# Kernel optimization log

Hardware: AMD Instinct MI355X
Metric: run time of the kernel (lower is better)

Reference implementation:

```python
import jax, jax.numpy as jnp
import numpy as np

B, S, D = 8, 1024, 768
H = 12
DH = D // H  # 64


def setup_inputs() -> dict:
    key = jax.random.key(0)
    ks = jax.random.split(key, 9)
    s = 0.02
    return {
        "x": jax.random.normal(ks[0], (B, S, D), dtype=jnp.float32),
        # per-head QKV projections stacked over heads: [H, D, DH]
        "Wq": jax.random.normal(ks[1], (H, D, DH), dtype=jnp.float32) * s,
        "bq": jax.random.normal(ks[2], (H, DH), dtype=jnp.float32) * s,
        "Wk": jax.random.normal(ks[3], (H, D, DH), dtype=jnp.float32) * s,
        "bk": jax.random.normal(ks[4], (H, DH), dtype=jnp.float32) * s,
        "Wv": jax.random.normal(ks[5], (H, D, DH), dtype=jnp.float32) * s,
        "bv": jax.random.normal(ks[6], (H, DH), dtype=jnp.float32) * s,
        # output projection: [D, D] (applied as x @ Wo + bo)
        "Wo": jax.random.normal(ks[7], (D, D), dtype=jnp.float32) * s,
        "bo": jax.random.normal(ks[8], (D,), dtype=jnp.float32) * s,
    }


def reference(x, Wq, bq, Wk, bk, Wv, bv, Wo, bo):
    # Per-head linear projections, vectorized over heads -> [B, H, S, DH]
    q = jnp.einsum("bsd,hde->bhse", x, Wq) + bq[None, :, None, :]
    k = jnp.einsum("bsd,hde->bhse", x, Wk) + bk[None, :, None, :]
    v = jnp.einsum("bsd,hde->bhse", x, Wv) + bv[None, :, None, :]
    scale = 1.0 / jnp.sqrt(jnp.asarray(DH, dtype=q.dtype))
    scores = jnp.einsum("bhse,bhte->bhst", q, k) * scale  # [B,H,S,S]
    probs = jax.nn.softmax(scores, axis=-1)  # dropout p=0 (eval)
    out = jnp.einsum("bhst,bhte->bhse", probs, v)  # [B,H,S,DH]
    # concat heads (head order matches ModuleList order) -> [B,S,D]
    out = out.transpose(0, 2, 1, 3).reshape(B, S, D)
    return out @ Wo + bo
```

## Files before the change

### kernel.cpp

```cpp
#include <hip/hip_runtime.h>
#include <math.h>

#define BB 8
#define SS 1024
#define DD 768
#define HH 12
#define DHH 64
#define BSS (BB*SS)
#define NQKV 2304
#define NT 24

typedef _Float16 half8 __attribute__((ext_vector_type(8)));
typedef _Float16 half4 __attribute__((ext_vector_type(4)));
typedef float    f32x4 __attribute__((ext_vector_type(4)));

__device__ __forceinline__ void glds16(const _Float16* g, _Float16* l)
{
    __builtin_amdgcn_global_load_lds(
        (const __attribute__((address_space(1))) uint32_t*)(g),
        (__attribute__((address_space(3))) uint32_t*)(l),
        16, 0, 0);
}

#define MF(a, b, c) __builtin_amdgcn_mfma_f32_16x16x32_f16(a, b, c, 0, 0, 0)

__global__ __launch_bounds__(256)
void prep(const float* __restrict__ x, _Float16* __restrict__ xh,
          const float* __restrict__ Wq, const float* __restrict__ Wk,
          const float* __restrict__ Wv, const float* __restrict__ Wo,
          _Float16* __restrict__ Wt, _Float16* __restrict__ Wot)
{
    const int blk = blockIdx.x;
    const int tid = threadIdx.x;

    if (blk < 3072) {
        int i = blk * 256 + tid;
        const float4* xp = (const float4*)x + (size_t)i * 2;
        float4 u = xp[0], v = xp[1];
        half8 h = { (_Float16)u.x, (_Float16)u.y, (_Float16)u.z, (_Float16)u.w,
                    (_Float16)v.x, (_Float16)v.y, (_Float16)v.z, (_Float16)v.w };
        ((half8*)xh)[i] = h;
        return;
    }

    __shared__ float T[64][65];
    const int t  = blk - 3072;
    const int z  = t / 144;
    const int r_ = t - z * 144;
    const int d0 = (r_ / 12) * 64;
    const int n_outer = r_ % 12;

    const float* src;
    _Float16* dst;
    int base_mul, row_stride;
    if (z < 3) {
        src = (z == 0) ? Wq : (z == 1) ? Wk : Wv;
        dst = Wt + (size_t)z * DD * DD;
        base_mul = DD * DHH; row_stride = DHH;
    } else {
        src = Wo; dst = Wot;
        base_mul = 64; row_stride = DD;
    }

    const size_t base = (size_t)n_outer * base_mul;
    {
        int dl = tid >> 2, c0 = (tid & 3) * 16;
        const float* p = src + base + (size_t)(d0 + dl) * row_stride + c0;
#pragma unroll
        for (int m = 0; m < 4; ++m) {
            float4 f = *(const float4*)(p + m * 4);
            T[dl][c0 + m*4 + 0] = f.x;
            T[dl][c0 + m*4 + 1] = f.y;
            T[dl][c0 + m*4 + 2] = f.z;
            T[dl][c0 + m*4 + 3] = f.w;
        }
    }
    __syncthreads();
    {
        int e = tid >> 2, c = tid & 3;
        half8 lo, hi;
#pragma unroll
        for (int i = 0; i < 8; ++i) {
            lo[i] = (_Float16)T[c*16 + i][e];
            hi[i] = (_Float16)T[c*16 + 8 + i][e];
        }
        _Float16* q = dst + ((size_t)n_outer * 64 + e) * DD + d0 + c * 16;
        *(half8*)q = lo;
        *(half8*)(q + 8) = hi;
    }
}

__global__ __launch_bounds__(512, 2)
void gemm_qkv_256(const _Float16* __restrict__ Xh, const _Float16* __restrict__ Wt,
                  const float* __restrict__ bq, const float* __restrict__ bk,
                  const float* __restrict__ bv,
                  _Float16* __restrict__ qo, _Float16* __restrict__ ko,
                  _Float16* __restrict__ vto)
{
    __shared__ _Float16 Ab[4][256][32];
    __shared__ _Float16 Bb[4][256][32];

    const int bid = blockIdx.x;
    const int c = bid & 7;
    const int g = bid >> 3;
    const int m0 = (c * 4 + g / 9) * 256;
    const int n0 = (g % 9) * 256;

    const int tid  = threadIdx.x;
    const int wave = tid >> 6;
    const int lane = tid & 63;
    const int l16  = tid & 15;
    const int quad = (tid >> 4) & 3;
    const int wy = wave >> 2;
    const int wx = wave & 3;

    const int scol = ((lane & 3) ^ ((lane >> 3) & 3)) * 8;
    const _Float16* ap0 = Xh + (size_t)(m0 + wave * 32 + (lane >> 2)) * DD + scol;
    const _Float16* bp0 = Wt + (size_t)(n0 + wave * 32 + (lane >> 2)) * DD + scol;

    const int fcol = (quad ^ ((l16 >> 1) & 3)) * 8;

    f32x4 acc[8][4];
#pragma unroll
    for (int i = 0; i < 8; ++i)
#pragma unroll
        for (int j = 0; j < 4; ++j) acc[i][j] = (f32x4){0.f, 0.f, 0.f, 0.f};

#pragma unroll
    for (int t = 0; t < 3; ++t) {
        glds16(ap0 + t * 32,           &Ab[t][wave * 32][0]);
        glds16(ap0 + t * 32 + 16 * DD, &Ab[t][wave * 32 + 16][0]);
        glds16(bp0 + t * 32,           &Bb[t][wave * 32][0]);
        glds16(bp0 + t * 32 + 16 * DD, &Bb[t][wave * 32 + 16][0]);
    }
    asm volatile("s_waitcnt vmcnt(8)\n\ts_barrier" ::: "memory");

#pragma unroll 4
    for (int kt = 0; kt < NT; ++kt) {
        const int bf = kt & 3;

        half8 a[8], bA[2];
#pragma unroll
        for (int i = 0; i < 8; ++i)
            a[i] = *(const half8*)&Ab[bf][wy * 128 + i * 16 + l16][fcol];
#pragma unroll
        for (int j = 0; j < 2; ++j)
            bA[j] = *(const half8*)&Bb[bf][wx * 64 + j * 16 + l16][fcol];
        if (kt + 3 < NT) {
            const int nf = (kt + 3) & 3;
            glds16(ap0 + (kt + 3) * 32,           &Ab[nf][wave * 32][0]);
            glds16(ap0 + (kt + 3) * 32 + 16 * DD, &Ab[nf][wave * 32 + 16][0]);
        }
        __builtin_amdgcn_s_setprio(1);
#pragma unroll
        for (int i = 0; i < 8; ++i) {
            acc[i][0] = MF(a[i], bA[0], acc[i][0]);
            acc[i][1] = MF(a[i], bA[1], acc[i][1]);
        }
        __builtin_amdgcn_s_setprio(0);

        half8 bB[2];
#pragma unroll
        for (int j = 0; j < 2; ++j)
            bB[j] = *(const half8*)&Bb[bf][wx * 64 + (2 + j) * 16 + l16][fcol];
        if (kt + 3 < NT) {
            const int nf = (kt + 3) & 3;
            glds16(bp0 + (kt + 3) * 32,           &Bb[nf][wave * 32][0]);
            glds16(bp0 + (kt + 3) * 32 + 16 * DD, &Bb[nf][wave * 32 + 16][0]);
        }
        __builtin_amdgcn_s_setprio(1);
#pragma unroll
        for (int i = 0; i < 8; ++i) {
            acc[i][2] = MF(a[i], bB[0], acc[i][2]);
            acc[i][3] = MF(a[i], bB[1], acc[i][3]);
        }
        __builtin_amdgcn_s_setprio(0);

        if (kt < NT - 3)
            asm volatile("s_waitcnt vmcnt(8)\n\ts_barrier" ::: "memory");
        else if (kt == NT - 3)
            asm volatile("s_waitcnt vmcnt(4)\n\ts_barrier" ::: "memory");
        else if (kt == NT - 2)
            asm volatile("s_waitcnt vmcnt(0)\n\ts_barrier" ::: "memory");
    }

    const int wsel  = n0 / 768;
    const int ncol0 = n0 - wsel * 768 + wx * 64;

    if (wsel == 0) {
#pragma unroll
        for (int i = 0; i < 8; ++i) {
#pragma unroll
            for (int r = 0; r < 4; ++r) {
                int row = m0 + wy * 128 + i * 16 + quad * 4 + r;
                int b_ = row >> 10;
                int s  = row & (SS - 1);
#pragma unroll
                for (int j = 0; j < 4; ++j) {
                    int nl = ncol0 + j * 16 + l16;
                    int h = nl >> 6, e = nl & 63;
                    float val = (acc[i][j][r] + bq[nl]) * 0.125f;
                    qo[((size_t)(b_ * HH + h) * SS + s) * DHH + e] = (_Float16)val;
                }
            }
        }
    } else if (wsel == 1) {
#pragma unroll
        for (int i = 0; i < 8; ++i) {
#pragma unroll
            for (int r = 0; r < 4; ++r) {
                int row = m0 + wy * 128 + i * 16 + quad * 4 + r;
                int b_ = row >> 10;
                int s  = row & (SS - 1);
#pragma unroll
                for (int j = 0; j < 4; ++j) {
                    int nl = ncol0 + j * 16 + l16;
                    int h = nl >> 6, e = nl & 63;
                    float val = acc[i][j][r] + bk[nl];
                    ko[((size_t)(b_ * HH + h) * SS + s) * DHH + e] = (_Float16)val;
                }
            }
        }
    } else {
#pragma unroll
        for (int i = 0; i < 8; ++i) {
#pragma unroll
            for (int r = 0; r < 4; ++r) {
                int row = m0 + wy * 128 + i * 16 + quad * 4 + r;
                int b_ = row >> 10;
                int s  = row & (SS - 1);
#pragma unroll
                for (int j = 0; j < 4; ++j) {
                    int nl = ncol0 + j * 16 + l16;
                    int h = nl >> 6, e = nl & 63;
                    float val = acc[i][j][r] + bv[nl];
                    vto[((size_t)(b_ * HH + h) * DHH + e) * SS + s] = (_Float16)val;
                }
            }
        }
    }
}

__global__ __launch_bounds__(256)
void gemm_out_f16(const _Float16* __restrict__ Ah, const _Float16* __restrict__ Bt,
                  const float* __restrict__ bias, float* __restrict__ out)
{
    __shared__ _Float16 Ash[2][128][32];
    __shared__ _Float16 Bsh[2][64][32];

    const int m0 = blockIdx.x * 128;
    const int n0 = blockIdx.y * 64;
    const int tid  = threadIdx.x;
    const int wave = tid >> 6;
    const int lane = tid & 63;
    const int l16  = tid & 15;
    const int quad = (tid >> 4) & 3;
    const int wy = wave >> 1;
    const int wx = wave & 1;

    const int scol = ((lane & 3) ^ ((lane >> 3) & 3)) * 8;
    const int fcol = (quad ^ ((l16 >> 1) & 3)) * 8;

    const _Float16* ap = Ah + (size_t)(m0 + 32 * wave + (lane >> 2)) * DD + scol;
    const _Float16* bp = Bt + (size_t)(n0 + 16 * wave + (lane >> 2)) * DD + scol;

    f32x4 acc[4][2];
#pragma unroll
    for (int i = 0; i < 4; ++i)
#pragma unroll
        for (int j = 0; j < 2; ++j) acc[i][j] = (f32x4){0.f, 0.f, 0.f, 0.f};

    glds16(ap, &Ash[0][32 * wave][0]);
    glds16(ap + 16 * DD, &Ash[0][32 * wave + 16][0]);
    glds16(bp, &Bsh[0][16 * wave][0]);

    int cur = 0;
    for (int k0 = 0; k0 < DD; k0 += 32) {
        __syncthreads();
        if (k0 + 32 < DD) {
            glds16(ap + k0 + 32, &Ash[cur ^ 1][32 * wave][0]);
            glds16(ap + k0 + 32 + 16 * DD, &Ash[cur ^ 1][32 * wave + 16][0]);
            glds16(bp + k0 + 32, &Bsh[cur ^ 1][16 * wave][0]);
        }

        half8 a[4], bf[2];
#pragma unroll
        for (int i = 0; i < 4; ++i)
            a[i] = *(const half8*)&Ash[cur][wy * 64 + i * 16 + l16][fcol];
#pragma unroll
        for (int j = 0; j < 2; ++j)
            bf[j] = *(const half8*)&Bsh[cur][wx * 32 + j * 16 + l16][fcol];
#pragma unroll
        for (int i = 0; i < 4; ++i)
#pragma unroll
            for (int j = 0; j < 2; ++j)
                acc[i][j] = MF(a[i], bf[j], acc[i][j]);
        cur ^= 1;
    }

#pragma unroll
    for (int i = 0; i < 4; ++i) {
#pragma unroll
        for (int r = 0; r < 4; ++r) {
            int row = m0 + wy * 64 + i * 16 + quad * 4 + r;
#pragma unroll
            for (int j = 0; j < 2; ++j) {
                int col = n0 + wx * 32 + j * 16 + l16;
                out[(size_t)row * DD + col] = acc[i][j][r] + bias[col];
            }
        }
    }
}

__global__ __launch_bounds__(256)
void attn_f16(const _Float16* __restrict__ qh, const _Float16* __restrict__ kh,
              const _Float16* __restrict__ vt, _Float16* __restrict__ ctxh)
{
    const int bh  = blockIdx.x;
    const int q0  = blockIdx.y * 128;
    const int tid = threadIdx.x;
    const int wave = tid >> 6;
    const int lane = tid & 63;
    const int l16  = tid & 15;
    const int quad = (tid >> 4) & 3;

    __shared__ _Float16 Ks[2][2][64][32];
    __shared__ _Float16 Vs[2][2][64][32];
    __shared__ _Float16 Pt[4][32][72];

    const int scol = ((lane & 3) ^ ((lane >> 3) & 3)) * 8;
    const int fcol = (quad ^ ((l16 >> 1) & 3)) * 8;

    const _Float16* qrow0 = qh + ((size_t)bh * SS + q0 + wave * 32 + l16) * DHH;
    const half8 qlo0 = *(const half8*)(qrow0 + quad * 8);
    const half8 qhi0 = *(const half8*)(qrow0 + 32 + quad * 8);
    const half8 qlo1 = *(const half8*)(qrow0 + 16 * DHH + quad * 8);
    const half8 qhi1 = *(const half8*)(qrow0 + 16 * DHH + 32 + quad * 8);

    const _Float16* kp = kh + ((size_t)bh * SS + 16 * wave + (lane >> 2)) * DHH + scol;
    const _Float16* vp = vt + ((size_t)bh * DHH + 16 * wave + (lane >> 2)) * SS + scol;

    f32x4 o0[4], o1[4];
    float lacc0 = 0.f, lacc1 = 0.f;
#pragma unroll
    for (int j = 0; j < 4; ++j) {
        o0[j] = (f32x4){0.f, 0.f, 0.f, 0.f};
        o1[j] = (f32x4){0.f, 0.f, 0.f, 0.f};
    }

    glds16(kp,      &Ks[0][0][16 * wave][0]);
    glds16(kp + 32, &Ks[0][1][16 * wave][0]);
    glds16(vp,      &Vs[0][0][16 * wave][0]);
    glds16(vp + 32, &Vs[0][1][16 * wave][0]);

    int cur = 0;
    for (int kt = 0; kt < SS; kt += 64) {
        __syncthreads();
        if (kt + 64 < SS) {
            glds16(kp + (size_t)(kt + 64) * DHH,      &Ks[cur ^ 1][0][16 * wave][0]);
            glds16(kp + (size_t)(kt + 64) * DHH + 32, &Ks[cur ^ 1][1][16 * wave][0]);
            glds16(vp + kt + 64,      &Vs[cur ^ 1][0][16 * wave][0]);
            glds16(vp + kt + 64 + 32, &Vs[cur ^ 1][1][16 * wave][0]);
        }

        f32x4 z0[4], z1[4];
#pragma unroll
        for (int f = 0; f < 4; ++f) {
            half8 klo = *(const half8*)&Ks[cur][0][f * 16 + l16][fcol];
            half8 khi = *(const half8*)&Ks[cur][1][f * 16 + l16][fcol];
            z0[f] = (f32x4){0.f, 0.f, 0.f, 0.f};
            z0[f] = MF(klo, qlo0, z0[f]);
            z0[f] = MF(khi, qhi0, z0[f]);
            z1[f] = (f32x4){0.f, 0.f, 0.f, 0.f};
            z1[f] = MF(klo, qlo1, z1[f]);
            z1[f] = MF(khi, qhi1, z1[f]);
        }

        half8 vv0[4], vv1[4];
#pragma unroll
        for (int j = 0; j < 4; ++j) {
            vv0[j] = *(const half8*)&Vs[cur][0][j * 16 + l16][fcol];
            vv1[j] = *(const half8*)&Vs[cur][1][j * 16 + l16][fcol];
        }

#pragma unroll
        for (int f = 0; f < 4; ++f) {
            half4 pk0, pk1;
#pragma unroll
            for (int r = 0; r < 4; ++r) {
                float p0 = __expf(z0[f][r]); lacc0 += p0; pk0[r] = (_Float16)p0;
                float p1 = __expf(z1[f][r]); lacc1 += p1; pk1[r] = (_Float16)p1;
            }
            *(half4*)&Pt[wave][l16][f * 16 + quad * 4]      = pk0;
            *(half4*)&Pt[wave][16 + l16][f * 16 + quad * 4] = pk1;
        }

        half8 pl0 = *(const half8*)&Pt[wave][l16][quad * 8];
        half8 ph0 = *(const half8*)&Pt[wave][l16][32 + quad * 8];
        half8 pl1 = *(const half8*)&Pt[wave][16 + l16][quad * 8];
        half8 ph1 = *(const half8*)&Pt[wave][16 + l16][32 + quad * 8];

#pragma unroll
        for (int j = 0; j < 4; ++j) {
            o0[j] = MF(pl0, vv0[j], o0[j]);
            o0[j] = MF(ph0, vv1[j], o0[j]);
            o1[j] = MF(pl1, vv0[j], o1[j]);
            o1[j] = MF(ph1, vv1[j], o1[j]);
        }
        cur ^= 1;
    }

    float lr0 = lacc0;
    lr0 += __shfl_xor(lr0, 16);
    lr0 += __shfl_xor(lr0, 32);
    float lr1 = lacc1;
    lr1 += __shfl_xor(lr1, 16);
    lr1 += __shfl_xor(lr1, 32);

    const int b_ = bh / HH;
    const int h_ = bh % HH;
#pragma unroll
    for (int r = 0; r < 4; ++r) {
        float inv0 = 1.f / __shfl(lr0, quad * 4 + r, 16);
        float inv1 = 1.f / __shfl(lr1, quad * 4 + r, 16);
        int s0_ = q0 + wave * 32 + quad * 4 + r;
        _Float16* orow0 = ctxh + ((size_t)(b_ * SS + s0_)) * DD + h_ * DHH;
        _Float16* orow1 = ctxh + ((size_t)(b_ * SS + s0_ + 16)) * DD + h_ * DHH;
#pragma unroll
        for (int j = 0; j < 4; ++j) {
            orow0[j * 16 + l16] = (_Float16)(o0[j][r] * inv0);
            orow1[j * 16 + l16] = (_Float16)(o1[j][r] * inv1);
        }
    }
}

extern "C" void kernel_launch(void* const* d_in, const int* in_sizes, int n_in,
                              void* d_out, int out_size, void* d_ws, size_t ws_size,
                              hipStream_t stream)
{
    const float* x  = (const float*)d_in[0];
    const float* Wq = (const float*)d_in[1];
    const float* bq = (const float*)d_in[2];
    const float* Wk = (const float*)d_in[3];
    const float* bk = (const float*)d_in[4];
    const float* Wv = (const float*)d_in[5];
    const float* bv = (const float*)d_in[6];
    const float* Wo = (const float*)d_in[7];
    const float* bo = (const float*)d_in[8];
    float* out = (float*)d_out;

    const size_t xe = (size_t)BSS * DD;
    const size_t we = (size_t)DD * DD;
    _Float16* Xh   = (_Float16*)d_ws;
    _Float16* Wt   = Xh  + xe;
    _Float16* Wot  = Wt  + (size_t)3 * we;
    _Float16* qhb  = Wot + we;
    _Float16* khb  = qhb + xe;
    _Float16* vtb  = khb + xe;
    _Float16* ctxh = vtb + xe;

    prep<<<3072 + 576, 256, 0, stream>>>(x, Xh, Wq, Wk, Wv, Wo, Wt, Wot);

    gemm_qkv_256<<<(BSS / 256) * (NQKV / 256), 512, 0, stream>>>(
        Xh, Wt, bq, bk, bv, qhb, khb, vtb);

    dim3 ag(BB * HH, SS / 128);
    attn_f16<<<ag, 256, 0, stream>>>(qhb, khb, vtb, ctxh);

    dim3 gg(BSS / 128, DD / 64);
    gemm_out_f16<<<gg, 256, 0, stream>>>(ctxh, Wot, bo, out);
}
```

Measured before the change: 205.1 us.

## Deepen output GEMM pipeline with 128x128 tiles; load attention K/V directly from global

The output-projection GEMM moves to 128x128 tiles with a 4-stage LDS ring buffer (3 tiles in flight), explicit vmcnt waits, setprio around the MFMA groups, and a swizzled 1-D block-to-tile mapping meant to improve L2 reuse. Separately, the attention kernel drops its LDS double-buffering of K and V and reads the fragments straight from global memory, which removes barriers but relies on cache hits across waves. The two changes pull in different directions: the GEMM is meant to get more reuse and overlap, while the attention path may lose bandwidth efficiency from uncoalesced 16-byte global reads.

New measurement: 252.7 us. 23.2% more time.

```diff
diff --git a/kernel.cpp b/kernel.cpp
--- a/kernel.cpp
+++ b/kernel.cpp
@@ -241,15 +241,19 @@
     }
 }
 
-__global__ __launch_bounds__(256)
+__global__ __launch_bounds__(256, 2)
 void gemm_out_f16(const _Float16* __restrict__ Ah, const _Float16* __restrict__ Bt,
                   const float* __restrict__ bias, float* __restrict__ out)
 {
-    __shared__ _Float16 Ash[2][128][32];
-    __shared__ _Float16 Bsh[2][64][32];
-
-    const int m0 = blockIdx.x * 128;
-    const int n0 = blockIdx.y * 64;
+    __shared__ _Float16 Ash[4][128][32];
+    __shared__ _Float16 Bsh[4][128][32];
+
+    const int bid = blockIdx.x;
+    const int c8  = bid & 7;
+    const int g   = bid >> 3;
+    const int m0 = (c8 * 8 + g / 6) * 128;
+    const int n0 = (g % 6) * 128;
+
     const int tid  = threadIdx.x;
     const int wave = tid >> 6;
     const int lane = tid & 63;
@@ -262,40 +266,70 @@
     const int fcol = (quad ^ ((l16 >> 1) & 3)) * 8;
 
     const _Float16* ap = Ah + (size_t)(m0 + 32 * wave + (lane >> 2)) * DD + scol;
-    const _Float16* bp = Bt + (size_t)(n0 + 16 * wave + (lane >> 2)) * DD + scol;
-
-    f32x4 acc[4][2];
+    const _Float16* bp = Bt + (size_t)(n0 + 32 * wave + (lane >> 2)) * DD + scol;
+
+    f32x4 acc[4][4];
 #pragma unroll
     for (int i = 0; i < 4; ++i)
 #pragma unroll
-        for (int j = 0; j < 2; ++j) acc[i][j] = (f32x4){0.f, 0.f, 0.f, 0.f};
-
-    glds16(ap, &Ash[0][32 * wave][0]);
-    glds16(ap + 16 * DD, &Ash[0][32 * wave + 16][0]);
-    glds16(bp, &Bsh[0][16 * wave][0]);
-
-    int cur = 0;
-    for (int k0 = 0; k0 < DD; k0 += 32) {
-        __syncthreads();
-        if (k0 + 32 < DD) {
-            glds16(ap + k0 + 32, &Ash[cur ^ 1][32 * wave][0]);
-            glds16(ap + k0 + 32 + 16 * DD, &Ash[cur ^ 1][32 * wave + 16][0]);
-            glds16(bp + k0 + 32, &Bsh[cur ^ 1][16 * wave][0]);
-        }
-
-        half8 a[4], bf[2];
+        for (int j = 0; j < 4; ++j) acc[i][j] = (f32x4){0.f, 0.f, 0.f, 0.f};
+
+#pragma unroll
+    for (int t = 0; t < 3; ++t) {
+        glds16(ap + t * 32,           &Ash[t][32 * wave][0]);
+        glds16(ap + t * 32 + 16 * DD, &Ash[t][32 * wave + 16][0]);
+        glds16(bp + t * 32,           &Bsh[t][32 * wave][0]);
+        glds16(bp + t * 32 + 16 * DD, &Bsh[t][32 * wave + 16][0]);
+    }
+    asm volatile("s_waitcnt vmcnt(8)\n\ts_barrier" ::: "memory");
+
+#pragma unroll 4
+    for (int kt = 0; kt < NT; ++kt) {
+        const int bf = kt & 3;
+
+        half8 a[4], bA[2];
 #pragma unroll
         for (int i = 0; i < 4; ++i)
-            a[i] = *(const half8*)&Ash[cur][wy * 64 + i * 16 + l16][fcol];
+            a[i] = *(const half8*)&Ash[bf][wy * 64 + i * 16 + l16][fcol];
 #pragma unroll
         for (int j = 0; j < 2; ++j)
-            bf[j] = *(const half8*)&Bsh[cur][wx * 32 + j * 16 + l16][fcol];
-#pragma unroll
-        for (int i = 0; i < 4; ++i)
-#pragma unroll
-            for (int j = 0; j < 2; ++j)
-                acc[i][j] = MF(a[i], bf[j], acc[i][j]);
-        cur ^= 1;
+            bA[j] = *(const half8*)&Bsh[bf][wx * 64 + j * 16 + l16][fcol];
+        if (kt + 3 < NT) {
+            const int nf = (kt + 3) & 3;
+            glds16(ap + (kt + 3) * 32,           &Ash[nf][32 * wave][0]);
+            glds16(ap + (kt + 3) * 32 + 16 * DD, &Ash[nf][32 * wave + 16][0]);
+        }
+        __builtin_amdgcn_s_setprio(1);
+#pragma unroll
+        for (int i = 0; i < 4; ++i) {
+            acc[i][0] = MF(a[i], bA[0], acc[i][0]);
+            acc[i][1] = MF(a[i], bA[1], acc[i][1]);
+        }
+        __builtin_amdgcn_s_setprio(0);
+
+        half8 bB[2];
+#pragma unroll
+        for (int j = 0; j < 2; ++j)
+            bB[j] = *(const half8*)&Bsh[bf][wx * 64 + (2 + j) * 16 + l16][fcol];
+        if (kt + 3 < NT) {
+            const int nf = (kt + 3) & 3;
+            glds16(bp + (kt + 3) * 32,           &Bsh[nf][32 * wave][0]);
+            glds16(bp + (kt + 3) * 32 + 16 * DD, &Bsh[nf][32 * wave + 16][0]);
+        }
+        __builtin_amdgcn_s_setprio(1);
+#pragma unroll
+        for (int i = 0; i < 4; ++i) {
+            acc[i][2] = MF(a[i], bB[0], acc[i][2]);
+            acc[i][3] = MF(a[i], bB[1], acc[i][3]);
+        }
+        __builtin_amdgcn_s_setprio(0);
+
+        if (kt < NT - 3)
+            asm volatile("s_waitcnt vmcnt(8)\n\ts_barrier" ::: "memory");
+        else if (kt == NT - 3)
+            asm volatile("s_waitcnt vmcnt(4)\n\ts_barrier" ::: "memory");
+        else if (kt == NT - 2)
+            asm volatile("s_waitcnt vmcnt(0)\n\ts_barrier" ::: "memory");
     }
 
 #pragma unroll
@@ -304,8 +338,8 @@
         for (int r = 0; r < 4; ++r) {
             int row = m0 + wy * 64 + i * 16 + quad * 4 + r;
 #pragma unroll
-            for (int j = 0; j < 2; ++j) {
-                int col = n0 + wx * 32 + j * 16 + l16;
+            for (int j = 0; j < 4; ++j) {
+                int col = n0 + wx * 64 + j * 16 + l16;
                 out[(size_t)row * DD + col] = acc[i][j][r] + bias[col];
             }
         }
@@ -320,16 +354,10 @@
     const int q0  = blockIdx.y * 128;
     const int tid = threadIdx.x;
     const int wave = tid >> 6;
-    const int lane = tid & 63;
     const int l16  = tid & 15;
     const int quad = (tid >> 4) & 3;
 
-    __shared__ _Float16 Ks[2][2][64][32];
-    __shared__ _Float16 Vs[2][2][64][32];
     __shared__ _Float16 Pt[4][32][72];
-
-    const int scol = ((lane & 3) ^ ((lane >> 3) & 3)) * 8;
-    const int fcol = (quad ^ ((l16 >> 1) & 3)) * 8;
 
     const _Float16* qrow0 = qh + ((size_t)bh * SS + q0 + wave * 32 + l16) * DHH;
     const half8 qlo0 = *(const half8*)(qrow0 + quad * 8);
@@ -337,8 +365,8 @@
     const half8 qlo1 = *(const half8*)(qrow0 + 16 * DHH + quad * 8);
     const half8 qhi1 = *(const half8*)(qrow0 + 16 * DHH + 32 + quad * 8);
 
-    const _Float16* kp = kh + ((size_t)bh * SS + 16 * wave + (lane >> 2)) * DHH + scol;
-    const _Float16* vp = vt + ((size_t)bh * DHH + 16 * wave + (lane >> 2)) * SS + scol;
+    const _Float16* kbase = kh + (size_t)bh * SS * DHH;
+    const _Float16* vbase = vt + (size_t)bh * DHH * SS;
 
     f32x4 o0[4], o1[4];
     float lacc0 = 0.f, lacc1 = 0.f;
@@ -348,26 +376,13 @@
         o1[j] = (f32x4){0.f, 0.f, 0.f, 0.f};
     }
 
-    glds16(kp,      &Ks[0][0][16 * wave][0]);
-    glds16(kp + 32, &Ks[0][1][16 * wave][0]);
-    glds16(vp,      &Vs[0][0][16 * wave][0]);
-    glds16(vp + 32, &Vs[0][1][16 * wave][0]);
-
-    int cur = 0;
     for (int kt = 0; kt < SS; kt += 64) {
-        __syncthreads();
-        if (kt + 64 < SS) {
-            glds16(kp + (size_t)(kt + 64) * DHH,      &Ks[cur ^ 1][0][16 * wave][0]);
-            glds16(kp + (size_t)(kt + 64) * DHH + 32, &Ks[cur ^ 1][1][16 * wave][0]);
-            glds16(vp + kt + 64,      &Vs[cur ^ 1][0][16 * wave][0]);
-            glds16(vp + kt + 64 + 32, &Vs[cur ^ 1][1][16 * wave][0]);
-        }
-
         f32x4 z0[4], z1[4];
 #pragma unroll
         for (int f = 0; f < 4; ++f) {
-            half8 klo = *(const half8*)&Ks[cur][0][f * 16 + l16][fcol];
-            half8 khi = *(const half8*)&Ks[cur][1][f * 16 + l16][fcol];
+            const _Float16* kr = kbase + (size_t)(kt + f * 16 + l16) * DHH + quad * 8;
+            half8 klo = *(const half8*)kr;
+            half8 khi = *(const half8*)(kr + 32);
             z0[f] = (f32x4){0.f, 0.f, 0.f, 0.f};
             z0[f] = MF(klo, qlo0, z0[f]);
             z0[f] = MF(khi, qhi0, z0[f]);
@@ -379,8 +394,9 @@
         half8 vv0[4], vv1[4];
 #pragma unroll
         for (int j = 0; j < 4; ++j) {
-            vv0[j] = *(const half8*)&Vs[cur][0][j * 16 + l16][fcol];
-            vv1[j] = *(const half8*)&Vs[cur][1][j * 16 + l16][fcol];
+            const _Float16* vr = vbase + (size_t)(j * 16 + l16) * SS + kt + quad * 8;
+            vv0[j] = *(const half8*)vr;
+            vv1[j] = *(const half8*)(vr + 32);
         }
 
 #pragma unroll
@@ -407,7 +423,6 @@
             o1[j] = MF(pl1, vv0[j], o1[j]);
             o1[j] = MF(ph1, vv1[j], o1[j]);
         }
-        cur ^= 1;
     }
 
     float lr0 = lacc0;
@@ -467,6 +482,5 @@
     dim3 ag(BB * HH, SS / 128);
     attn_f16<<<ag, 256, 0, stream>>>(qhb, khb, vtb, ctxh);
 
-    dim3 gg(BSS / 128, DD / 64);
-    gemm_out_f16<<<gg, 256, 0, stream>>>(ctxh, Wot, bo, out);
-}
+    gemm_out_f16<<<(BSS / 128) * (DD / 128), 256, 0, stream>>>(ctxh, Wot, bo, out);
+}
```
